# Optimization experiments

Measured on AMD Instinct MI355X. Metric: run time of the kernel, lower is better.

The kernel has to match this reference:

```python
import jax, jax.numpy as jnp
import numpy as np

IN, OUT, RANK, ORDER, BATCH = 1024, 1024, 32, 3, 4096


def setup_inputs() -> dict:
    key = jax.random.key(0)
    ks = jax.random.split(key, 16)
    inp = {}
    inp['X'] = jax.random.normal(ks[0], (BATCH, IN), dtype=jnp.float32)
    inp['const'] = jnp.zeros((OUT,), dtype=jnp.float32)
    for i in range(ORDER):
        # Taylor-style scales: keep magnitudes controlled for higher orders
        o_std = (1.0 / RANK) ** 0.5 if i == 0 else 0.01
        inp[f'O{i}'] = o_std * jax.random.normal(ks[1 + i], (OUT, RANK), dtype=jnp.float32)
        base = 1.0
        for t in range(i + 1):
            base = base / (RANK + 2 * t)
        i_std = base ** (1.0 / 2 ** (i + 1))
        inp[f'I{i}'] = i_std * jax.random.normal(ks[4 + i], (i + 1, RANK, IN), dtype=jnp.float32)
        g_std = (1.0 / RANK ** (i + 1)) ** 0.5
        inp[f'G{i}'] = g_std * jax.random.normal(ks[7 + i], (RANK, RANK ** (i + 1)), dtype=jnp.float32)
    return inp


def _taylor_forward(X, const, Os, Is, Gs):
    # X: (batch, in). X0 = 0.0 so no shift needed beyond subtracting 0.
    batch = X.shape[0]
    rank = Is[0].shape[1]
    Y = jnp.broadcast_to(const[None, :], (batch, const.shape[0]))
    for i in range(len(Os)):
        # Z[j] = I[j] @ X.T -> (i+1, rank, batch)
        Z = jnp.einsum('jri,bi->jrb', Is[i], X)
        kron = Z[0]  # (rank, batch)
        for j in range(1, i + 1):
            # broadcasted outer product, matching torch loop order:
            # result[z_j, z_{j-1}, ..., z_0, batch]
            X3 = Z[j].reshape((rank,) + (1,) * j + (batch,))
            kron = kron[None] * X3
        kron = kron.reshape((-1, batch))  # (rank**(i+1), batch)
        Y = Y + (Os[i] @ (Gs[i] @ kron)).T
    return Y


def reference(X, const, O0, O1, O2, I0, I1, I2, G0, G1, G2):
    return _taylor_forward(X, const, [O0, O1, O2], [I0, I1, I2], [G0, G1, G2])
```

## Files before the change

### kernel.cpp

```cpp
#include <hip/hip_runtime.h>


typedef float f4 __attribute__((ext_vector_type(4)));
typedef _Float16 h8 __attribute__((ext_vector_type(8)));
typedef _Float16 h4 __attribute__((ext_vector_type(4)));
typedef unsigned int u32x4 __attribute__((ext_vector_type(4)));

#define ZH_OFF  0u
#define TH_OFF  1572864u
#define OCH_OFF 2097152u
#define G2H_OFF 2293760u

__device__ __forceinline__ h8 splat8(unsigned int u) {
    _Float16 s = __builtin_bit_cast(_Float16, (unsigned short)(u & 0xffffu));
    return h8{ s, s, s, s, s, s, s, s };
}

__device__ __forceinline__ void stage_bcast16(const _Float16* zsrc, unsigned int* dst) {
    u32x4 u0 = *(const u32x4*)zsrc;
    u32x4 u1 = *(const u32x4*)(zsrc + 8);
    #pragma unroll
    for (int k = 0; k < 4; ++k) {
        dst[2*k]       = (u0[k] & 0xffffu) * 0x00010001u;
        dst[2*k + 1]   = (u0[k] >> 16)     * 0x00010001u;
        dst[8 + 2*k]   = (u1[k] & 0xffffu) * 0x00010001u;
        dst[8 + 2*k+1] = (u1[k] >> 16)     * 0x00010001u;
    }
}

__global__ __launch_bounds__(512) void prep_gemmx(
    const float* __restrict__ X,
    const float* __restrict__ I0, const float* __restrict__ I1, const float* __restrict__ I2,
    const float* __restrict__ O0, const float* __restrict__ O1, const float* __restrict__ O2,
    const float* __restrict__ G0, const float* __restrict__ G2,
    _Float16* __restrict__ Och, _Float16* __restrict__ G2h, _Float16* __restrict__ Z)
{
    const int bx = blockIdx.x;
    const int t = threadIdx.x;
    if (bx >= 192) {
        if (bx < 704) {
            int i = ((bx - 192) * 512 + t) * 4;
            f4 v = *(const f4*)(G2 + i);
            h4 o = { (_Float16)v[0], (_Float16)v[1], (_Float16)v[2], (_Float16)v[3] };
            *(h4*)(G2h + i) = o;
        } else {
            int idx = (bx - 704) * 512 + t;
            int o = idx / 96, j = idx - o * 96;
            float v;
            if (j < 32) {
                v = 0.f;
                #pragma unroll
                for (int q = 0; q < 32; ++q) v += O0[o*32 + q] * G0[q*32 + j];
            } else if (j < 64) v = O1[o*32 + (j - 32)];
            else               v = O2[o*32 + (j - 64)];
            Och[idx] = (_Float16)v;
        }
        return;
    }
    __shared__ _Float16 As[2][2][64 * 64];
    __shared__ _Float16 Bs[2][2][64 * 64];
    const int g  = t >> 8;
    const int tt = t & 255;
    const int work = (bx & 7) * 24 + (bx >> 3);
    const int m0 = (work / 3) * 64, n0 = (work % 3) * 64;
    const int wid = tt >> 6, lane = tt & 63;
    const int wr = wid >> 1, wc = wid & 1;
    const int lr = lane & 15, lg = lane >> 4;
    const int arow = tt >> 2, aq = tt & 3;

    const float* xbase = X + (size_t)(m0 + arow) * 1024 + g * 512 + aq * 16;
    const int wrow = n0 + arow;
    const float* wbase = (wrow < 32) ? I0 + (size_t)wrow * 1024
                       : (wrow < 96) ? I1 + (size_t)(wrow - 32) * 1024
                                     : I2 + (size_t)(wrow - 96) * 1024;
    wbase += g * 512 + aq * 16;
    const int sw0 = arow * 64 + (((aq * 2)     ^ (arow & 7)) << 3);
    const int sw1 = arow * 64 + (((aq * 2 + 1) ^ (arow & 7)) << 3);

    f4 xa[2][4], wa[2][4];
    #define LOADX(set, step) { \
        const float* xp = xbase + (step) * 64; \
        const float* wp = wbase + (step) * 64; \
        _Pragma("unroll") \
        for (int q = 0; q < 4; ++q) { xa[set][q] = *(const f4*)(xp + q*4); wa[set][q] = *(const f4*)(wp + q*4); } }
    #define STAGE(set, buf) { \
        h8 ha0, ha1, hb0, hb1; \
        _Pragma("unroll") \
        for (int j = 0; j < 4; ++j) { \
            ha0[j] = (_Float16)xa[set][0][j]; ha0[4+j] = (_Float16)xa[set][1][j]; \
            ha1[j] = (_Float16)xa[set][2][j]; ha1[4+j] = (_Float16)xa[set][3][j]; \
            hb0[j] = (_Float16)wa[set][0][j]; hb0[4+j] = (_Float16)wa[set][1][j]; \
            hb1[j] = (_Float16)wa[set][2][j]; hb1[4+j] = (_Float16)wa[set][3][j]; \
        } \
        *(h8*)&As[g][buf][sw0] = ha0; *(h8*)&As[g][buf][sw1] = ha1; \
        *(h8*)&Bs[g][buf][sw0] = hb0; *(h8*)&Bs[g][buf][sw1] = hb1; }

    LOADX(0, 0); LOADX(1, 1);
    STAGE(0, 0);
    LOADX(0, 2);

    f4 acc[2][2];
    #pragma unroll
    for (int mt = 0; mt < 2; ++mt)
        #pragma unroll
        for (int nt = 0; nt < 2; ++nt) acc[mt][nt] = f4{0.f,0.f,0.f,0.f};

    #pragma unroll
    for (int s = 0; s < 8; ++s) {
        const int cur = s & 1;
        __syncthreads();
        if (s < 7) STAGE((s + 1) & 1, cur ^ 1);
        if (s < 5) LOADX((s + 1) & 1, s + 3);
        #pragma unroll
        for (int ks = 0; ks < 2; ++ks) {
            h8 av[2], bv[2];
            #pragma unroll
            for (int mt = 0; mt < 2; ++mt) {
                int row = wr * 32 + mt * 16 + lr, gg = ks * 4 + lg;
                av[mt] = *(const h8*)&As[g][cur][row * 64 + ((gg ^ (row & 7)) << 3)];
            }
            #pragma unroll
            for (int nt = 0; nt < 2; ++nt) {
                int row = wc * 32 + nt * 16 + lr, gg = ks * 4 + lg;
                bv[nt] = *(const h8*)&Bs[g][cur][row * 64 + ((gg ^ (row & 7)) << 3)];
            }
            #pragma unroll
            for (int mt = 0; mt < 2; ++mt)
                #pragma unroll
                for (int nt = 0; nt < 2; ++nt)
                    acc[mt][nt] = __builtin_amdgcn_mfma_f32_16x16x32_f16(av[mt], bv[nt], acc[mt][nt], 0, 0, 0);
        }
    }
    #undef LOADX
    #undef STAGE
    __syncthreads();
    float* Red = (float*)&As[0][0][0];
    if (g == 1) {
        #pragma unroll
        for (int mt = 0; mt < 2; ++mt)
            #pragma unroll
            for (int nt = 0; nt < 2; ++nt)
                #pragma unroll
                for (int i = 0; i < 4; ++i)
                    Red[tt * 16 + mt * 8 + nt * 4 + i] = acc[mt][nt][i];
    }
    __syncthreads();
    if (g == 0) {
        #pragma unroll
        for (int mt = 0; mt < 2; ++mt)
            #pragma unroll
            for (int nt = 0; nt < 2; ++nt)
                #pragma unroll
                for (int i = 0; i < 4; ++i)
                    Z[(size_t)(m0 + wr*32 + mt*16 + lg*4 + i) * 192 + n0 + wc*32 + nt*16 + lr]
                        = (_Float16)(acc[mt][nt][i] + Red[tt * 16 + mt * 8 + nt * 4 + i]);
    }
}

__global__ __launch_bounds__(256) void kron_fused(
    const _Float16* __restrict__ Z, const _Float16* __restrict__ G2h,
    const float* __restrict__ G1, _Float16* __restrict__ T)
{
    __shared__ __align__(16) unsigned char smem[37376];
    unsigned int* Zs1 = (unsigned int*)smem;
    _Float16* Bs = (_Float16*)(smem + 16896);
    const int bx = blockIdx.x;
    const int t = threadIdx.x;
    const int wid = t >> 6, lane = t & 63;
    const int lr = lane & 15, lg = lane >> 4;
    const bool is_t2 = bx < 512;
    const int m0 = is_t2 ? (bx >> 4) * 128 : (bx - 512) * 128;
    const int zcol = is_t2 ? 128 : 64;

    {
        int row = t >> 1, c0 = (t & 1) * 16;
        stage_bcast16(Z + (size_t)(m0 + row) * 192 + zcol + c0, Zs1 + row * 33 + c0);
    }

    if (is_t2) {
        const int n0 = (bx & 15) * 64;
        const int wm0 = (wid >> 1) * 64, wn0 = (wid & 1) * 32;
        h8 a0v[4];
        #pragma unroll
        for (int mt = 0; mt < 4; ++mt)
            a0v[mt] = *(const h8*)(Z + (size_t)(m0 + wm0 + mt*16 + lr) * 192 + 96 + lg * 8);

        f4 acc[4][2];
        #pragma unroll
        for (int mt = 0; mt < 4; ++mt)
            #pragma unroll
            for (int nt = 0; nt < 2; ++nt) acc[mt][nt] = f4{0.f, 0.f, 0.f, 0.f};

        const int brow = t >> 2, bg = t & 3;
        const f4* gsrc = (const f4*)(G2h + (size_t)(n0 + brow) * 1024 + bg * 8);
        f4 brA[2], brB[2];
        brA[0] = gsrc[0];  brB[0] = gsrc[4];
        {
            *(f4*)&Bs[0 * 5120 + 0 * 2560 + brow * 40 + bg * 8] = brA[0];
            *(f4*)&Bs[0 * 5120 + 1 * 2560 + brow * 40 + bg * 8] = brB[0];
        }
        brA[1] = gsrc[8];  brB[1] = gsrc[12];
        brA[0] = gsrc[16]; brB[0] = gsrc[20];

        unsigned int zu[2][2][4];
        #pragma unroll
        for (int i = 0; i < 16; ++i) {
            const int cur = i & 1;
            __syncthreads();
            if (i == 0) {
                #pragma unroll
                for (int q = 0; q < 2; ++q)
                    #pragma unroll
                    for (int mt = 0; mt < 4; ++mt)
                        zu[0][q][mt] = Zs1[(wm0 + mt*16 + lr) * 33 + q];
            }
            if (i < 15) {
                const int set = (i + 1) & 1;
                *(f4*)&Bs[(cur ^ 1) * 5120 + 0 * 2560 + brow * 40 + bg * 8] = brA[set];
                *(f4*)&Bs[(cur ^ 1) * 5120 + 1 * 2560 + brow * 40 + bg * 8] = brB[set];
                #pragma unroll
                for (int q = 0; q < 2; ++q)
                    #pragma unroll
                    for (int mt = 0; mt < 4; ++mt)
                        zu[set][q][mt] = Zs1[(wm0 + mt*16 + lr) * 33 + 2*(i+1) + q];
            }
            if (i < 13) {
                const int set = (i + 1) & 1;
                brA[set] = gsrc[(i + 3) * 8];
                brB[set] = gsrc[(i + 3) * 8 + 4];
            }
            #pragma unroll
            for (int q = 0; q < 2; ++q) {
                h8 bf0 = *(const h8*)&Bs[cur * 5120 + q * 2560 + (wn0 + lr) * 40 + lg * 8];
                h8 bf1 = *(const h8*)&Bs[cur * 5120 + q * 2560 + (wn0 + 16 + lr) * 40 + lg * 8];
                #pragma unroll
                for (int mt = 0; mt < 4; ++mt) {
                    h8 z1b = splat8(zu[cur][q][mt]);
                    h8 af = z1b * a0v[mt];
                    acc[mt][0] = __builtin_amdgcn_mfma_f32_16x16x32_f16(af, bf0, acc[mt][0], 0, 0, 0);
                    acc[mt][1] = __builtin_amdgcn_mfma_f32_16x16x32_f16(af, bf1, acc[mt][1], 0, 0, 0);
                }
            }
        }

        __syncthreads();
        float* Ms = (float*)smem;
        #pragma unroll
        for (int mt = 0; mt < 4; ++mt)
            #pragma unroll
            for (int nt = 0; nt < 2; ++nt)
                #pragma unroll
                for (int i = 0; i < 4; ++i)
                    Ms[(wm0 + mt*16 + lg*4 + i) * 66 + wn0 + nt*16 + lr] = acc[mt][nt][i];
        __syncthreads();
        {
            int row = t >> 1, rl = t & 1;
            const _Float16* z2p = Z + (size_t)(m0 + row) * 192 + 160;
            const float* mrow = Ms + row * 66 + rl * 32;
            float sum = 0.f;
            #pragma unroll
            for (int r2 = 0; r2 < 32; ++r2) sum += mrow[r2] * (float)z2p[r2];
            T[(size_t)(m0 + row) * 64 + 32 + (bx & 15) * 2 + rl] = (_Float16)sum;
        }
    } else {
        h8 a0v[2];
        #pragma unroll
        for (int mt = 0; mt < 2; ++mt)
            a0v[mt] = *(const h8*)(Z + (size_t)(m0 + wid*32 + mt*16 + lr) * 192 + 32 + lg * 8);

        const int brow = t >> 3, bq = (t & 7) * 4;
        const float* g1src = G1 + (size_t)brow * 1024 + bq;
        f4 bw = *(const f4*)g1src;
        {
            h4 bh = { (_Float16)bw[0], (_Float16)bw[1], (_Float16)bw[2], (_Float16)bw[3] };
            *(h4*)&Bs[brow * 40 + bq] = bh;
        }
        bw = *(const f4*)(g1src + 32);

        f4 acc[2][2];
        #pragma unroll
        for (int mt = 0; mt < 2; ++mt)
            #pragma unroll
            for (int nt = 0; nt < 2; ++nt) acc[mt][nt] = f4{0.f,0.f,0.f,0.f};
        __syncthreads();

        for (int s = 0; s < 32; ++s) {
            const int cur = s & 1;
            if (s < 31) {
                h4 bh = { (_Float16)bw[0], (_Float16)bw[1], (_Float16)bw[2], (_Float16)bw[3] };
                *(h4*)&Bs[(cur ^ 1) * 1280 + brow * 40 + bq] = bh;
            }
            if (s < 30) bw = *(const f4*)(g1src + (s + 2) * 32);
            h8 bf[2];
            #pragma unroll
            for (int nt = 0; nt < 2; ++nt)
                bf[nt] = *(const h8*)&Bs[cur * 1280 + (nt*16 + lr) * 40 + lg * 8];
            #pragma unroll
            for (int mt = 0; mt < 2; ++mt) {
                h8 z1b = splat8(Zs1[(wid*32 + mt*16 + lr) * 33 + s]);
                h8 af = z1b * a0v[mt];
                acc[mt][0] = __builtin_amdgcn_mfma_f32_16x16x32_f16(af, bf[0], acc[mt][0], 0, 0, 0);
                acc[mt][1] = __builtin_amdgcn_mfma_f32_16x16x32_f16(af, bf[1], acc[mt][1], 0, 0, 0);
            }
            __syncthreads();
        }
        #pragma unroll
        for (int mt = 0; mt < 2; ++mt)
            #pragma unroll
            for (int nt = 0; nt < 2; ++nt)
                #pragma unroll
                for (int i = 0; i < 4; ++i)
                    T[(size_t)(m0 + wid*32 + mt*16 + lg*4 + i) * 64 + nt*16 + lr]
                        = (_Float16)acc[mt][nt][i];
    }
}

__global__ __launch_bounds__(256) void gemm_y_mfma(
    const _Float16* __restrict__ Z, const _Float16* __restrict__ T,
    const _Float16* __restrict__ Och, const float* __restrict__ cst,
    float* __restrict__ Y)
{
    __shared__ _Float16 As[64 * 104];
    __shared__ _Float16 Bs[128 * 104];
    const int t = threadIdx.x;
    const int n0 = blockIdx.x * 128, m0 = blockIdx.y * 64;
    {
        int row = t >> 2, seg = t & 3;
        const _Float16* zp = Z + (size_t)(m0 + row) * 192;
        const _Float16* tp = T + (size_t)(m0 + row) * 64;
        _Float16* dst = As + row * 104;
        if (seg == 0) {
            *(h8*)(dst)      = *(const h8*)(zp);
            *(h8*)(dst + 8)  = *(const h8*)(zp + 8);
            *(h8*)(dst + 16) = *(const h8*)(zp + 16);
        } else if (seg == 1) {
            *(h8*)(dst + 24) = *(const h8*)(zp + 24);
            *(h8*)(dst + 32) = *(const h8*)(tp);
            *(h8*)(dst + 40) = *(const h8*)(tp + 8);
        } else if (seg == 2) {
            *(h8*)(dst + 48) = *(const h8*)(tp + 16);
            *(h8*)(dst + 56) = *(const h8*)(tp + 24);
            *(h8*)(dst + 64) = *(const h8*)(tp + 32);
        } else {
            *(h8*)(dst + 72) = *(const h8*)(tp + 40);
            *(h8*)(dst + 80) = *(const h8*)(tp + 48);
            *(h8*)(dst + 88) = *(const h8*)(tp + 56);
        }
        int row2 = t >> 1, half = t & 1;
        const _Float16* src = Och + (size_t)(n0 + row2) * 96 + half * 48;
        _Float16* bdst = Bs + row2 * 104 + half * 48;
        #pragma unroll
        for (int q = 0; q < 6; ++q) *(h8*)(bdst + q * 8) = *(const h8*)(src + q * 8);
    }
    const int wid = t >> 6, lane = t & 63;
    const int wvr = wid >> 1, wvc = wid & 1;
    const int lr = lane & 15, lg = lane >> 4;
    float bias[4];
    #pragma unroll
    for (int nt = 0; nt < 4; ++nt) bias[nt] = cst[n0 + wvc*64 + nt*16 + lr];
    __syncthreads();

    f4 acc[2][4];
    #pragma unroll
    for (int mt = 0; mt < 2; ++mt)
        #pragma unroll
        for (int nt = 0; nt < 4; ++nt) acc[mt][nt] = f4{0.f,0.f,0.f,0.f};

    #pragma unroll
    for (int ks = 0; ks < 3; ++ks) {
        h8 av[2], bv[4];
        #pragma unroll
        for (int mt = 0; mt < 2; ++mt)
            av[mt] = *(const h8*)&As[(wvr*32 + mt*16 + lr) * 104 + ks*32 + lg*8];
        #pragma unroll
        for (int nt = 0; nt < 4; ++nt)
            bv[nt] = *(const h8*)&Bs[(wvc*64 + nt*16 + lr) * 104 + ks*32 + lg*8];
        #pragma unroll
        for (int mt = 0; mt < 2; ++mt)
            #pragma unroll
            for (int nt = 0; nt < 4; ++nt)
                acc[mt][nt] = __builtin_amdgcn_mfma_f32_16x16x32_f16(av[mt], bv[nt], acc[mt][nt], 0, 0, 0);
    }
    #pragma unroll
    for (int mt = 0; mt < 2; ++mt)
        #pragma unroll
        for (int nt = 0; nt < 4; ++nt)
            #pragma unroll
            for (int i = 0; i < 4; ++i)
                Y[(size_t)(m0 + wvr*32 + mt*16 + lg*4 + i) * 1024 + n0 + wvc*64 + nt*16 + lr]
                    = acc[mt][nt][i] + bias[nt];
}

extern "C" void kernel_launch(void* const* d_in, const int* in_sizes, int n_in,
                              void* d_out, int out_size, void* d_ws, size_t ws_size,
                              hipStream_t stream) {
    const float* X   = (const float*)d_in[0];
    const float* cst = (const float*)d_in[1];
    const float* O0  = (const float*)d_in[2];
    const float* I0  = (const float*)d_in[3];
    const float* G0  = (const float*)d_in[4];
    const float* O1  = (const float*)d_in[5];
    const float* I1  = (const float*)d_in[6];
    const float* G1  = (const float*)d_in[7];
    const float* O2  = (const float*)d_in[8];
    const float* I2  = (const float*)d_in[9];
    const float* G2  = (const float*)d_in[10];
    unsigned char* ws = (unsigned char*)d_ws;
    _Float16* Zh  = (_Float16*)(ws + ZH_OFF);
    _Float16* Th  = (_Float16*)(ws + TH_OFF);
    _Float16* Oh  = (_Float16*)(ws + OCH_OFF);
    _Float16* G2h = (_Float16*)(ws + G2H_OFF);
    float* Y = (float*)d_out;

    prep_gemmx<<<896, 512, 0, stream>>>(X, I0, I1, I2, O0, O1, O2, G0, G2, Oh, G2h, Zh);
    kron_fused<<<544, 256, 0, stream>>>(Zh, G2h, G1, Th);
    gemm_y_mfma<<<dim3(8, 64), 256, 0, stream>>>(Zh, Th, Oh, cst, Y);
}
```

Before: 36.52 us.

## Split kron_fused K-loop across two thread groups with shared-memory reduction

Doubles the kron_fused block to 512 threads and splits the reduction dimension between two 256-thread groups, each with its own shared-memory B buffers and half the loop iterations. The partial accumulators are combined through a shared-memory reduction before the epilogue. This shortens each block's serial K-loop and raises in-block parallelism. The cost is more shared memory per block, which may lower occupancy, plus extra barriers and reduction traffic.

```diff
diff --git a/kernel.cpp b/kernel.cpp
--- a/kernel.cpp
+++ b/kernel.cpp
@@ -157,22 +157,23 @@
     }
 }
 
-__global__ __launch_bounds__(256) void kron_fused(
+__global__ __launch_bounds__(512) void kron_fused(
     const _Float16* __restrict__ Z, const _Float16* __restrict__ G2h,
     const float* __restrict__ G1, _Float16* __restrict__ T)
 {
-    __shared__ __align__(16) unsigned char smem[37376];
+    __shared__ __align__(16) unsigned char smem[57856];
     unsigned int* Zs1 = (unsigned int*)smem;
     _Float16* Bs = (_Float16*)(smem + 16896);
     const int bx = blockIdx.x;
     const int t = threadIdx.x;
-    const int wid = t >> 6, lane = t & 63;
+    const int g = t >> 8, tt = t & 255;
+    const int wid = tt >> 6, lane = tt & 63;
     const int lr = lane & 15, lg = lane >> 4;
     const bool is_t2 = bx < 512;
     const int m0 = is_t2 ? (bx >> 4) * 128 : (bx - 512) * 128;
     const int zcol = is_t2 ? 128 : 64;
 
-    {
+    if (t < 256) {
         int row = t >> 1, c0 = (t & 1) * 16;
         stage_bcast16(Z + (size_t)(m0 + row) * 192 + zcol + c0, Zs1 + row * 33 + c0);
     }
@@ -191,20 +192,21 @@
             #pragma unroll
             for (int nt = 0; nt < 2; ++nt) acc[mt][nt] = f4{0.f, 0.f, 0.f, 0.f};
 
-        const int brow = t >> 2, bg = t & 3;
-        const f4* gsrc = (const f4*)(G2h + (size_t)(n0 + brow) * 1024 + bg * 8);
+        const int brow = tt >> 2, bg = tt & 3;
+        const f4* gsrc = (const f4*)(G2h + (size_t)(n0 + brow) * 1024 + g * 512 + bg * 8);
+        _Float16* BsG = Bs + g * 10240;
         f4 brA[2], brB[2];
         brA[0] = gsrc[0];  brB[0] = gsrc[4];
         {
-            *(f4*)&Bs[0 * 5120 + 0 * 2560 + brow * 40 + bg * 8] = brA[0];
-            *(f4*)&Bs[0 * 5120 + 1 * 2560 + brow * 40 + bg * 8] = brB[0];
+            *(f4*)&BsG[0 * 5120 + 0 * 2560 + brow * 40 + bg * 8] = brA[0];
+            *(f4*)&BsG[0 * 5120 + 1 * 2560 + brow * 40 + bg * 8] = brB[0];
         }
         brA[1] = gsrc[8];  brB[1] = gsrc[12];
         brA[0] = gsrc[16]; brB[0] = gsrc[20];
 
         unsigned int zu[2][2][4];
         #pragma unroll
-        for (int i = 0; i < 16; ++i) {
+        for (int i = 0; i < 8; ++i) {
             const int cur = i & 1;
             __syncthreads();
             if (i == 0) {
@@ -212,27 +214,27 @@
                 for (int q = 0; q < 2; ++q)
                     #pragma unroll
                     for (int mt = 0; mt < 4; ++mt)
-                        zu[0][q][mt] = Zs1[(wm0 + mt*16 + lr) * 33 + q];
-            }
-            if (i < 15) {
+                        zu[0][q][mt] = Zs1[(wm0 + mt*16 + lr) * 33 + 16*g + q];
+            }
+            if (i < 7) {
                 const int set = (i + 1) & 1;
-                *(f4*)&Bs[(cur ^ 1) * 5120 + 0 * 2560 + brow * 40 + bg * 8] = brA[set];
-                *(f4*)&Bs[(cur ^ 1) * 5120 + 1 * 2560 + brow * 40 + bg * 8] = brB[set];
+                *(f4*)&BsG[(cur ^ 1) * 5120 + 0 * 2560 + brow * 40 + bg * 8] = brA[set];
+                *(f4*)&BsG[(cur ^ 1) * 5120 + 1 * 2560 + brow * 40 + bg * 8] = brB[set];
                 #pragma unroll
                 for (int q = 0; q < 2; ++q)
                     #pragma unroll
                     for (int mt = 0; mt < 4; ++mt)
-                        zu[set][q][mt] = Zs1[(wm0 + mt*16 + lr) * 33 + 2*(i+1) + q];
-            }
-            if (i < 13) {
+                        zu[set][q][mt] = Zs1[(wm0 + mt*16 + lr) * 33 + 16*g + 2*(i+1) + q];
+            }
+            if (i < 5) {
                 const int set = (i + 1) & 1;
                 brA[set] = gsrc[(i + 3) * 8];
                 brB[set] = gsrc[(i + 3) * 8 + 4];
             }
             #pragma unroll
             for (int q = 0; q < 2; ++q) {
-                h8 bf0 = *(const h8*)&Bs[cur * 5120 + q * 2560 + (wn0 + lr) * 40 + lg * 8];
-                h8 bf1 = *(const h8*)&Bs[cur * 5120 + q * 2560 + (wn0 + 16 + lr) * 40 + lg * 8];
+                h8 bf0 = *(const h8*)&BsG[cur * 5120 + q * 2560 + (wn0 + lr) * 40 + lg * 8];
+                h8 bf1 = *(const h8*)&BsG[cur * 5120 + q * 2560 + (wn0 + 16 + lr) * 40 + lg * 8];
                 #pragma unroll
                 for (int mt = 0; mt < 4; ++mt) {
                     h8 z1b = splat8(zu[cur][q][mt]);
@@ -244,16 +246,39 @@
         }
 
         __syncthreads();
+        float* Red = (float*)(smem + 16896);
+        if (g == 1) {
+            #pragma unroll
+            for (int mt = 0; mt < 4; ++mt)
+                #pragma unroll
+                for (int nt = 0; nt < 2; ++nt)
+                    #pragma unroll
+                    for (int i = 0; i < 4; ++i)
+                        Red[tt * 32 + (mt * 2 + nt) * 4 + i] = acc[mt][nt][i];
+        }
+        __syncthreads();
+        if (g == 0) {
+            #pragma unroll
+            for (int mt = 0; mt < 4; ++mt)
+                #pragma unroll
+                for (int nt = 0; nt < 2; ++nt)
+                    #pragma unroll
+                    for (int i = 0; i < 4; ++i)
+                        acc[mt][nt][i] += Red[tt * 32 + (mt * 2 + nt) * 4 + i];
+        }
+        __syncthreads();
         float* Ms = (float*)smem;
-        #pragma unroll
-        for (int mt = 0; mt < 4; ++mt)
-            #pragma unroll
-            for (int nt = 0; nt < 2; ++nt)
-                #pragma unroll
-                for (int i = 0; i < 4; ++i)
-                    Ms[(wm0 + mt*16 + lg*4 + i) * 66 + wn0 + nt*16 + lr] = acc[mt][nt][i];
-        __syncthreads();
-        {
+        if (g == 0) {
+            #pragma unroll
+            for (int mt = 0; mt < 4; ++mt)
+                #pragma unroll
+                for (int nt = 0; nt < 2; ++nt)
+                    #pragma unroll
+                    for (int i = 0; i < 4; ++i)
+                        Ms[(wm0 + mt*16 + lg*4 + i) * 66 + wn0 + nt*16 + lr] = acc[mt][nt][i];
+        }
+        __syncthreads();
+        if (t < 256) {
             int row = t >> 1, rl = t & 1;
             const _Float16* z2p = Z + (size_t)(m0 + row) * 192 + 160;
             const float* mrow = Ms + row * 66 + rl * 32;
@@ -268,12 +293,13 @@
         for (int mt = 0; mt < 2; ++mt)
             a0v[mt] = *(const h8*)(Z + (size_t)(m0 + wid*32 + mt*16 + lr) * 192 + 32 + lg * 8);
 
-        const int brow = t >> 3, bq = (t & 7) * 4;
-        const float* g1src = G1 + (size_t)brow * 1024 + bq;
+        const int brow = tt >> 3, bq = (tt & 7) * 4;
+        const float* g1src = G1 + (size_t)brow * 1024 + g * 512 + bq;
+        _Float16* BsG = Bs + g * 2560;
         f4 bw = *(const f4*)g1src;
         {
             h4 bh = { (_Float16)bw[0], (_Float16)bw[1], (_Float16)bw[2], (_Float16)bw[3] };
-            *(h4*)&Bs[brow * 40 + bq] = bh;
+            *(h4*)&BsG[brow * 40 + bq] = bh;
         }
         bw = *(const f4*)(g1src + 32);
 
@@ -284,34 +310,47 @@
             for (int nt = 0; nt < 2; ++nt) acc[mt][nt] = f4{0.f,0.f,0.f,0.f};
         __syncthreads();
 
-        for (int s = 0; s < 32; ++s) {
+        for (int s = 0; s < 16; ++s) {
             const int cur = s & 1;
-            if (s < 31) {
+            if (s < 15) {
                 h4 bh = { (_Float16)bw[0], (_Float16)bw[1], (_Float16)bw[2], (_Float16)bw[3] };
-                *(h4*)&Bs[(cur ^ 1) * 1280 + brow * 40 + bq] = bh;
-            }
-            if (s < 30) bw = *(const f4*)(g1src + (s + 2) * 32);
+                *(h4*)&BsG[(cur ^ 1) * 1280 + brow * 40 + bq] = bh;
+            }
+            if (s < 14) bw = *(const f4*)(g1src + (s + 2) * 32);
             h8 bf[2];
             #pragma unroll
             for (int nt = 0; nt < 2; ++nt)
-                bf[nt] = *(const h8*)&Bs[cur * 1280 + (nt*16 + lr) * 40 + lg * 8];
+                bf[nt] = *(const h8*)&BsG[cur * 1280 + (nt*16 + lr) * 40 + lg * 8];
             #pragma unroll
             for (int mt = 0; mt < 2; ++mt) {
-                h8 z1b = splat8(Zs1[(wid*32 + mt*16 + lr) * 33 + s]);
+                h8 z1b = splat8(Zs1[(wid*32 + mt*16 + lr) * 33 + 16*g + s]);
                 h8 af = z1b * a0v[mt];
                 acc[mt][0] = __builtin_amdgcn_mfma_f32_16x16x32_f16(af, bf[0], acc[mt][0], 0, 0, 0);
                 acc[mt][1] = __builtin_amdgcn_mfma_f32_16x16x32_f16(af, bf[1], acc[mt][1], 0, 0, 0);
             }
             __syncthreads();
         }
-        #pragma unroll
-        for (int mt = 0; mt < 2; ++mt)
-            #pragma unroll
-            for (int nt = 0; nt < 2; ++nt)
-                #pragma unroll
-                for (int i = 0; i < 4; ++i)
-                    T[(size_t)(m0 + wid*32 + mt*16 + lg*4 + i) * 64 + nt*16 + lr]
-                        = (_Float16)acc[mt][nt][i];
+        float* Red = (float*)smem;
+        if (g == 1) {
+            #pragma unroll
+            for (int mt = 0; mt < 2; ++mt)
+                #pragma unroll
+                for (int nt = 0; nt < 2; ++nt)
+                    #pragma unroll
+                    for (int i = 0; i < 4; ++i)
+                        Red[tt * 16 + (mt * 2 + nt) * 4 + i] = acc[mt][nt][i];
+        }
+        __syncthreads();
+        if (g == 0) {
+            #pragma unroll
+            for (int mt = 0; mt < 2; ++mt)
+                #pragma unroll
+                for (int nt = 0; nt < 2; ++nt)
+                    #pragma unroll
+                    for (int i = 0; i < 4; ++i)
+                        T[(size_t)(m0 + wid*32 + mt*16 + lg*4 + i) * 64 + nt*16 + lr]
+                            = (_Float16)(acc[mt][nt][i] + Red[tt * 16 + (mt * 2 + nt) * 4 + i]);
+        }
     }
 }
 
@@ -413,6 +452,6 @@
     float* Y = (float*)d_out;
 
     prep_gemmx<<<896, 512, 0, stream>>>(X, I0, I1, I2, O0, O1, O2, G0, G2, Oh, G2h, Zh);
-    kron_fused<<<544, 256, 0, stream>>>(Zh, G2h, G1, Th);
+    kron_fused<<<544, 512, 0, stream>>>(Zh, G2h, G1, Th);
     gemm_y_mfma<<<dim3(8, 64), 256, 0, stream>>>(Zh, Th, Oh, cst, Y);
 }
```

New measurement: 40.95 us. 12.1% more time.
